# Optimization experiments

Hardware: AMD Instinct MI355X
Metric: run time of the kernel (lower is better)

The kernel has to match this reference:

```python
import jax, jax.numpy as jnp
import numpy as np


def _proj_prelu(x, W, b, a):
    # 1x1 conv (pointwise linear over channels) + PReLU with scalar slope
    y = jnp.einsum('nchw,oc->nohw', x, W) + b[None, :, None, None]
    return jnp.where(y >= 0, y, a[0] * y)


def setup_inputs() -> dict:
    key = jax.random.key(0)
    ks = jax.random.split(key, 8)
    C, Ce = 128, 64
    x = jax.random.normal(ks[0], (4, C, 80, 80), dtype=jnp.float32)
    s = 1.0 / np.sqrt(C)
    Wq = jax.random.normal(ks[1], (Ce, C), dtype=jnp.float32) * s
    bq = jax.random.normal(ks[2], (Ce,), dtype=jnp.float32) * 0.01
    Wk = jax.random.normal(ks[3], (Ce, C), dtype=jnp.float32) * s
    bk = jax.random.normal(ks[4], (Ce,), dtype=jnp.float32) * 0.01
    Wv = jax.random.normal(ks[5], (C, C), dtype=jnp.float32) * s
    bv = jax.random.normal(ks[6], (C,), dtype=jnp.float32) * 0.01
    aq = jnp.full((1,), 0.25, dtype=jnp.float32)
    ak = jnp.full((1,), 0.25, dtype=jnp.float32)
    av = jnp.full((1,), 0.25, dtype=jnp.float32)
    return {'x': x, 'Wq': Wq, 'bq': bq, 'aq': aq, 'Wk': Wk, 'bk': bk,
            'ak': ak, 'Wv': Wv, 'bv': bv, 'av': av}


def reference(x, Wq, bq, aq, Wk, bk, ak, Wv, bv, av):
    q = _proj_prelu(x, Wq, bq, aq)   # [N, Ce, H, W]
    k = _proj_prelu(x, Wk, bk, ak)   # [N, Ce, H, W]
    v = _proj_prelu(x, Wv, bv, av)   # [N, C,  H, W]
    N, Ce, H, W = q.shape
    Cv = v.shape[1]
    HW = H * W
    qf = q.reshape(N, Ce, HW)        # torch permute+view -> [N, HW, Ce] = qf^T
    kf = k.reshape(N, Ce, HW)
    vf = v.reshape(N, Cv, HW)
    score = jnp.einsum('nci,ncj->nij', qf, kf)      # [N, HW, HW]
    attn = jax.nn.softmax(score, axis=2)
    out = jnp.einsum('nij,ncj->nci', attn, vf)      # [N, Cv, HW]
    return out.reshape(N, Cv, H, W)
```

## Files before the change

### kernel.cpp

```cpp
#include <hip/hip_runtime.h>

typedef __attribute__((ext_vector_type(8)))  short bf16x8;
typedef __attribute__((ext_vector_type(16))) float f32x16;
typedef unsigned int u32;
typedef unsigned short u16;

#define HW 6400
#define L2E 1.44269504088896f
#define DEFER_THR 8.0f

__device__ inline u16 f2bf(float f) {
    u32 u = __builtin_bit_cast(u32, f);
    u32 r = (u + 0x7fffu + ((u >> 16) & 1u)) >> 16;
    return (u16)r;
}
__device__ inline u32 cvt_pk_bf16(float lo, float hi) {
    u32 r;
    asm("v_cvt_pk_bf16_f32 %0, %1, %2" : "=v"(r) : "v"(lo), "v"(hi));
    return r;
}
__device__ inline void gload_lds16(const void* g, void* l) {
    __builtin_amdgcn_global_load_lds(
        (const __attribute__((address_space(1))) u32*)g,
        (__attribute__((address_space(3))) u32*)l, 16, 0, 0);
}
__device__ inline float vmax16(const f32x16& v) {
    float a0 = fmaxf(v[0], v[1]),  a1 = fmaxf(v[2], v[3]);
    float a2 = fmaxf(v[4], v[5]),  a3 = fmaxf(v[6], v[7]);
    float a4 = fmaxf(v[8], v[9]),  a5 = fmaxf(v[10], v[11]);
    float a6 = fmaxf(v[12], v[13]), a7 = fmaxf(v[14], v[15]);
    float b0 = fmaxf(a0, a1), b1 = fmaxf(a2, a3);
    float b2 = fmaxf(a4, a5), b3 = fmaxf(a6, a7);
    return fmaxf(fmaxf(b0, b1), fmaxf(b2, b3));
}
__device__ inline float bfpair_sum(u32 w) {
    float hi = __builtin_bit_cast(float, w & 0xFFFF0000u);
    float lo = __builtin_bit_cast(float, w << 16);
    return hi + lo;
}

__global__ __launch_bounds__(256) void proj_kernel(
    const float* __restrict__ x,
    const float* __restrict__ Wq, const float* __restrict__ bq, const float* __restrict__ aq,
    const float* __restrict__ Wk, const float* __restrict__ bk, const float* __restrict__ ak,
    const float* __restrict__ Wv, const float* __restrict__ bv, const float* __restrict__ av,
    u16* __restrict__ QT, u16* __restrict__ KT, u16* __restrict__ Vw)
{
    __shared__ char xs[64 * 272];
    __shared__ char ktr[2][64 * 144];

    const int tid  = threadIdx.x;
    const int lane = tid & 63;
    const int w    = tid >> 6;
    const int l31  = lane & 31;
    const int h    = lane >> 5;

    const int blk = blockIdx.x;
    const int n   = blk / 100;
    const int pt  = blk - n * 100;
    const int p0  = pt * 64;

    const float* xb = x + (size_t)n * 128 * HW + p0;
    #pragma unroll
    for (int it = 0; it < 8; ++it) {
        int idx = it * 256 + tid;
        int c = idx >> 4, p4 = (idx & 15) * 4;
        float4 d = *(const float4*)(xb + (size_t)c * HW + p4);
        *(u16*)(xs + (p4 + 0) * 272 + c * 2) = f2bf(d.x);
        *(u16*)(xs + (p4 + 1) * 272 + c * 2) = f2bf(d.y);
        *(u16*)(xs + (p4 + 2) * 272 + c * 2) = f2bf(d.z);
        *(u16*)(xs + (p4 + 3) * 272 + c * 2) = f2bf(d.w);
    }
    __syncthreads();

    const float* Wsrc; const float* bsrc; float slope; float osc = 1.0f;
    if (w == 0)      { Wsrc = Wq;                 bsrc = bq;             slope = aq[0]; osc = L2E; }
    else if (w == 1) { Wsrc = Wk;                 bsrc = bk;             slope = ak[0]; }
    else             { Wsrc = Wv + (w-2)*64*128;  bsrc = bv + (w-2)*64;  slope = av[0]; }

    bf16x8 wf[2][8];
    #pragma unroll
    for (int cb = 0; cb < 2; ++cb)
        #pragma unroll
        for (int kc = 0; kc < 8; ++kc) {
            const float* ws = Wsrc + (cb * 32 + l31) * 128 + kc * 16 + h * 8;
            float4 a = *(const float4*)ws;
            float4 b = *(const float4*)(ws + 4);
            union { u32 u[4]; bf16x8 v; } uu;
            uu.u[0] = cvt_pk_bf16(a.x, a.y);
            uu.u[1] = cvt_pk_bf16(a.z, a.w);
            uu.u[2] = cvt_pk_bf16(b.x, b.y);
            uu.u[3] = cvt_pk_bf16(b.z, b.w);
            wf[cb][kc] = uu.v;
        }

    f32x16 acc[2][2] = {};
    #pragma unroll
    for (int kc = 0; kc < 8; ++kc) {
        bf16x8 xb0 = *(const bf16x8*)(xs + (l31)      * 272 + kc * 32 + h * 16);
        bf16x8 xb1 = *(const bf16x8*)(xs + (l31 + 32) * 272 + kc * 32 + h * 16);
        acc[0][0] = __builtin_amdgcn_mfma_f32_32x32x16_bf16(wf[0][kc], xb0, acc[0][0], 0, 0, 0);
        acc[0][1] = __builtin_amdgcn_mfma_f32_32x32x16_bf16(wf[0][kc], xb1, acc[0][1], 0, 0, 0);
        acc[1][0] = __builtin_amdgcn_mfma_f32_32x32x16_bf16(wf[1][kc], xb0, acc[1][0], 0, 0, 0);
        acc[1][1] = __builtin_amdgcn_mfma_f32_32x32x16_bf16(wf[1][kc], xb1, acc[1][1], 0, 0, 0);
    }

    if (w >= 2) {
        u16* dst = Vw + ((size_t)n * 128 + (size_t)(w - 2) * 64) * HW;
        #pragma unroll
        for (int cb = 0; cb < 2; ++cb)
            #pragma unroll
            for (int pb = 0; pb < 2; ++pb)
                #pragma unroll
                for (int r = 0; r < 16; ++r) {
                    int ch = cb * 32 + (r & 3) + 8 * (r >> 2) + 4 * h;
                    float y = acc[cb][pb][r] + bsrc[ch];
                    y = (y >= 0.f) ? y : slope * y;
                    dst[(size_t)ch * HW + p0 + pb * 32 + l31] = f2bf(y);
                }
    } else {
        char* tb = ktr[w];
        #pragma unroll
        for (int cb = 0; cb < 2; ++cb)
            #pragma unroll
            for (int pb = 0; pb < 2; ++pb)
                #pragma unroll
                for (int rp = 0; rp < 8; ++rp) {
                    int r0 = rp * 2;
                    int ch = cb * 32 + (r0 & 3) + 8 * (r0 >> 2) + 4 * h;
                    float y0 = acc[cb][pb][r0]     + bsrc[ch];
                    float y1 = acc[cb][pb][r0 + 1] + bsrc[ch + 1];
                    y0 = ((y0 >= 0.f) ? y0 : slope * y0) * osc;
                    y1 = ((y1 >= 0.f) ? y1 : slope * y1) * osc;
                    *(u32*)(tb + (pb * 32 + l31) * 144 + ch * 2) = cvt_pk_bf16(y0, y1);
                }
        u16* dst = (w == 0) ? QT : KT;
        #pragma unroll
        for (int i8 = 0; i8 < 8; ++i8) {
            int p = i8 * 8 + (lane >> 3);
            bf16x8 d = *(const bf16x8*)(tb + p * 144 + (lane & 7) * 16);
            *(bf16x8*)(dst + ((size_t)n * HW + p0 + p) * 64 + (lane & 7) * 8) = d;
        }
    }
}

__global__ __launch_bounds__(256, 2) void attn_kernel(
    const u16* __restrict__ QT, const u16* __restrict__ KT, const u16* __restrict__ Vw,
    float* __restrict__ out,
    float* __restrict__ Opart, float* __restrict__ Mpart, float* __restrict__ Lpart,
    int jsplit, int NT)
{
    __shared__ char lds[49152];

    const int tid  = threadIdx.x;
    const int lane = tid & 63;
    const int w    = tid >> 6;
    const int l31  = lane & 31;
    const int h    = lane >> 5;

    const int per_n = 25 * jsplit;
    const int n    = blockIdx.x / per_n;
    const int rem  = blockIdx.x - n * per_n;
    const int it   = rem / jsplit;
    const int js   = rem - it * jsplit;
    const int i0   = it * 256;
    const int jt0  = js * NT;

    const int rowA = i0 + w * 64 + l31;
    const int rowB = rowA + 32;

    const u16* qbA = QT + ((size_t)n * HW + rowA) * 64;
    bf16x8 qfA[4], qfB[4];
    #pragma unroll
    for (int kc = 0; kc < 4; ++kc) {
        qfA[kc] = *(const bf16x8*)(qbA + kc * 16 + h * 8);
        qfB[kc] = *(const bf16x8*)(qbA + 32 * 64 + kc * 16 + h * 8);
    }

    const char* Kg = (const char*)(KT + (size_t)n * HW * 64);
    const char* Vg = (const char*)(Vw + (size_t)n * 128 * HW);

    auto stage = [&](int buf, int jt) {
        char* B = lds + buf * 24576;
        #pragma unroll
        for (int q = 0; q < 2; ++q) {
            int cc = w + 4 * q;
            gload_lds16(Kg + (size_t)jt * 8192 + lane * 128 + cc * 16, B + cc * 1024);
        }
        #pragma unroll
        for (int q = 0; q < 4; ++q) {
            int v = w + 4 * q;
            int jcc = v >> 1, chalf = v & 1;
            gload_lds16(Vg + (size_t)(chalf * 64 + lane) * 12800 + (size_t)jt * 128 + jcc * 16,
                        B + 8192 + v * 1024);
        }
    };

    f32x16 accA[4] = {}, accB[4] = {};
    float mA = -3e38f, mB = -3e38f, lsA = 0.f, lsB = 0.f;

    auto compute = [&](int buf) {
        char* Klds = lds + buf * 24576;
        char* Vlds = Klds + 8192;

        #pragma unroll
        for (int jb = 0; jb < 2; ++jb) {
            bf16x8 kf[4];
            #pragma unroll
            for (int kc = 0; kc < 4; ++kc)
                kf[kc] = *(const bf16x8*)(Klds + (2 * kc + h) * 1024 + (jb * 32 + l31) * 16);

            __builtin_amdgcn_s_setprio(1);
            f32x16 sA = {}, sB = {};
            #pragma unroll
            for (int kc = 0; kc < 4; ++kc) {
                sA = __builtin_amdgcn_mfma_f32_32x32x16_bf16(kf[kc], qfA[kc], sA, 0, 0, 0);
                sB = __builtin_amdgcn_mfma_f32_32x32x16_bf16(kf[kc], qfB[kc], sB, 0, 0, 0);
            }
            __builtin_amdgcn_s_setprio(0);

            float rmxA = vmax16(sA), rmxB = vmax16(sB);
            rmxA = fmaxf(rmxA, __shfl_xor(rmxA, 32, 64));
            rmxB = fmaxf(rmxB, __shfl_xor(rmxB, 32, 64));

            if (__any(rmxA > mA + DEFER_THR)) {
                float mn = fmaxf(mA, rmxA);
                float a = exp2f(mA - mn);
                lsA *= a;
                #pragma unroll
                for (int cb = 0; cb < 4; ++cb)
                    #pragma unroll
                    for (int r = 0; r < 16; ++r) accA[cb][r] *= a;
                mA = mn;
            }
            if (__any(rmxB > mB + DEFER_THR)) {
                float mn = fmaxf(mB, rmxB);
                float a = exp2f(mB - mn);
                lsB *= a;
                #pragma unroll
                for (int cb = 0; cb < 4; ++cb)
                    #pragma unroll
                    for (int r = 0; r < 16; ++r) accB[cb][r] *= a;
                mB = mn;
            }

            #pragma unroll
            for (int r = 0; r < 16; ++r) {
                sA[r] = exp2f(sA[r] - mA);
                sB[r] = exp2f(sB[r] - mB);
            }

            float rsA = 0.f, rsB = 0.f;
            bf16x8 pfA[2], pfB[2];
            #pragma unroll
            for (int kbl = 0; kbl < 2; ++kbl) {
                const int b = kbl * 8;
                u32 a0 = cvt_pk_bf16(sA[b + 0], sA[b + 1]);
                u32 a1 = cvt_pk_bf16(sA[b + 2], sA[b + 3]);
                u32 a2 = cvt_pk_bf16(sA[b + 4], sA[b + 5]);
                u32 a3 = cvt_pk_bf16(sA[b + 6], sA[b + 7]);
                rsA += (bfpair_sum(a0) + bfpair_sum(a1)) + (bfpair_sum(a2) + bfpair_sum(a3));
                asm("v_permlane32_swap_b32 %0, %1" : "+v"(a0), "+v"(a2));
                asm("v_permlane32_swap_b32 %0, %1" : "+v"(a1), "+v"(a3));
                union { u32 u[4]; bf16x8 v; } ua;
                ua.u[0] = a0; ua.u[1] = a1; ua.u[2] = a2; ua.u[3] = a3;
                pfA[kbl] = ua.v;
                u32 b0 = cvt_pk_bf16(sB[b + 0], sB[b + 1]);
                u32 b1 = cvt_pk_bf16(sB[b + 2], sB[b + 3]);
                u32 b2 = cvt_pk_bf16(sB[b + 4], sB[b + 5]);
                u32 b3 = cvt_pk_bf16(sB[b + 6], sB[b + 7]);
                rsB += (bfpair_sum(b0) + bfpair_sum(b1)) + (bfpair_sum(b2) + bfpair_sum(b3));
                asm("v_permlane32_swap_b32 %0, %1" : "+v"(b0), "+v"(b2));
                asm("v_permlane32_swap_b32 %0, %1" : "+v"(b1), "+v"(b3));
                union { u32 u[4]; bf16x8 v; } ub;
                ub.u[0] = b0; ub.u[1] = b1; ub.u[2] = b2; ub.u[3] = b3;
                pfB[kbl] = ub.v;
            }
            lsA += rsA;
            lsB += rsB;

            __builtin_amdgcn_s_setprio(1);
            #pragma unroll
            for (int kbl = 0; kbl < 2; ++kbl) {
                const int jcc = jb * 4 + 2 * kbl + h;
                #pragma unroll
                for (int cb = 0; cb < 4; ++cb) {
                    bf16x8 vf = *(const bf16x8*)(Vlds + jcc * 2048 + (cb * 32 + l31) * 16);
                    accA[cb] = __builtin_amdgcn_mfma_f32_32x32x16_bf16(vf, pfA[kbl], accA[cb], 0, 0, 0);
                    accB[cb] = __builtin_amdgcn_mfma_f32_32x32x16_bf16(vf, pfB[kbl], accB[cb], 0, 0, 0);
                }
            }
            __builtin_amdgcn_s_setprio(0);
        }
    };

    #define WAITBAR(N) do { \
        asm volatile("s_waitcnt vmcnt(" #N ")" ::: "memory"); \
        __builtin_amdgcn_s_barrier(); \
        __builtin_amdgcn_sched_barrier(0); \
    } while (0)
    #define BAR() do { \
        __builtin_amdgcn_sched_barrier(0); \
        __builtin_amdgcn_s_barrier(); \
        __builtin_amdgcn_sched_barrier(0); \
    } while (0)

    stage(0, jt0);
    int t = 0;
    for (; t + 2 <= NT; t += 2) {
        stage(1, jt0 + t + 1);
        WAITBAR(6);
        compute(0);
        BAR();
        if (t + 2 < NT) {
            stage(0, jt0 + t + 2);
            WAITBAR(6);
        } else {
            WAITBAR(0);
        }
        compute(1);
        BAR();
    }
    if (t < NT) {
        asm volatile("s_waitcnt vmcnt(0)" ::: "memory");
        __builtin_amdgcn_s_barrier();
        __builtin_amdgcn_sched_barrier(0);
        compute(0);
    }
    #undef WAITBAR
    #undef BAR

    lsA += __shfl_xor(lsA, 32, 64);
    lsB += __shfl_xor(lsB, 32, 64);

    if (Opart != nullptr) {
        float* Ob = Opart + (size_t)(js * 4 + n) * 128 * HW;
        #pragma unroll
        for (int cb = 0; cb < 4; ++cb)
            #pragma unroll
            for (int r = 0; r < 16; ++r) {
                int c = cb * 32 + (r & 3) + 8 * (r >> 2) + 4 * h;
                Ob[(size_t)c * HW + rowA] = accA[cb][r];
                Ob[(size_t)c * HW + rowB] = accB[cb][r];
            }
        if (h == 0) {
            Mpart[(size_t)(js * 4 + n) * HW + rowA] = mA;
            Mpart[(size_t)(js * 4 + n) * HW + rowB] = mB;
            Lpart[(size_t)(js * 4 + n) * HW + rowA] = lsA;
            Lpart[(size_t)(js * 4 + n) * HW + rowB] = lsB;
        }
    } else {
        float invA = 1.f / lsA, invB = 1.f / lsB;
        float* ob = out + (size_t)n * 128 * HW;
        #pragma unroll
        for (int cb = 0; cb < 4; ++cb)
            #pragma unroll
            for (int r = 0; r < 16; ++r) {
                int c = cb * 32 + (r & 3) + 8 * (r >> 2) + 4 * h;
                ob[(size_t)c * HW + rowA] = accA[cb][r] * invA;
                ob[(size_t)c * HW + rowB] = accB[cb][r] * invB;
            }
    }
}

__global__ __launch_bounds__(256) void combine_kernel(
    const float* __restrict__ Opart, const float* __restrict__ Mpart,
    const float* __restrict__ Lpart, float* __restrict__ out, int jsplit)
{
    const int b = blockIdx.x;
    const int n = b / 100;
    const int rem = b - n * 100;
    const int cq = rem / 25;
    const int ic = rem - cq * 25;
    const int i = ic * 256 + threadIdx.x;

    float mj[5], wj[5];
    float M = -3e38f;
    #pragma unroll
    for (int js = 0; js < 5; ++js) {
        mj[js] = (js < jsplit) ? Mpart[(size_t)(js * 4 + n) * HW + i] : -3e38f;
        M = fmaxf(M, mj[js]);
    }
    float L = 0.f;
    #pragma unroll
    for (int js = 0; js < 5; ++js) {
        wj[js] = (js < jsplit) ? exp2f(mj[js] - M) : 0.f;
        if (js < jsplit) L += Lpart[(size_t)(js * 4 + n) * HW + i] * wj[js];
    }
    const float inv = 1.f / L;

    for (int c = cq * 32; c < cq * 32 + 32; ++c) {
        float acc = 0.f;
        #pragma unroll
        for (int js = 0; js < 5; ++js)
            if (js < jsplit)
                acc += Opart[((size_t)(js * 4 + n) * 128 + c) * HW + i] * wj[js];
        out[((size_t)n * 128 + c) * HW + i] = acc * inv;
    }
}

extern "C" void kernel_launch(void* const* d_in, const int* in_sizes, int n_in,
                              void* d_out, int out_size, void* d_ws, size_t ws_size,
                              hipStream_t stream) {
    const float* x  = (const float*)d_in[0];
    const float* Wq = (const float*)d_in[1];
    const float* bq = (const float*)d_in[2];
    const float* aq = (const float*)d_in[3];
    const float* Wk = (const float*)d_in[4];
    const float* bk = (const float*)d_in[5];
    const float* ak = (const float*)d_in[6];
    const float* Wv = (const float*)d_in[7];
    const float* bv = (const float*)d_in[8];
    const float* av = (const float*)d_in[9];

    char* wsp = (char*)d_ws;
    u16* QT  = (u16*)wsp;
    u16* KT  = (u16*)(wsp + 3276800);
    u16* Vw  = (u16*)(wsp + 6553600);
    const size_t base = 13107200;
    const size_t oslab = 13107200;
    const size_t mslab = 102400;

    proj_kernel<<<dim3(400), 256, 0, stream>>>(x, Wq, bq, aq, Wk, bk, ak, Wv, bv, av,
                                               QT, KT, Vw);

    int jsplit = 0;
    for (int js = 5; js >= 4; --js) {
        size_t need = base + (size_t)js * (oslab + 2 * mslab);
        if (ws_size >= need) { jsplit = js; break; }
    }

    if (jsplit > 0) {
        float* Opart = (float*)(wsp + base);
        float* Mpart = (float*)(wsp + base + (size_t)jsplit * oslab);
        float* Lpart = (float*)(wsp + base + (size_t)jsplit * (oslab + mslab));
        int NT = 100 / jsplit;
        attn_kernel<<<dim3(4 * 25 * jsplit), 256, 0, stream>>>(QT, KT, Vw, (float*)d_out,
                                                               Opart, Mpart, Lpart, jsplit, NT);
        combine_kernel<<<dim3(400), 256, 0, stream>>>(Opart, Mpart, Lpart, (float*)d_out, jsplit);
    } else {
        attn_kernel<<<dim3(100), 256, 0, stream>>>(QT, KT, Vw, (float*)d_out,
                                                   nullptr, nullptr, nullptr, 1, 100);
    }
}
```

Before: 167.0 us.

## Use raw exp2 intrinsic, sum fp32 probabilities directly, retune LDS pitches

Replaces exp2f with the hardware exp2 intrinsic in the attention and combine kernels, which drops the denormal/range fixup code around each exponential. The row sum is now taken from the fp32 probabilities instead of unpacking the bf16-packed pairs. The LDS row pitches in the projection kernel change from 272/144 to 260/132 bytes to alter the bank mapping. The new pitches are not multiples of 16, so the 16-byte vector LDS reads lose alignment. The row sum may also differ slightly from the bf16 values actually fed to the PV matmul.

New measurement: 143.7 us. 1.16x faster.

```diff
diff --git a/kernel.cpp b/kernel.cpp
--- a/kernel.cpp
+++ b/kernel.cpp
@@ -8,6 +8,8 @@
 #define HW 6400
 #define L2E 1.44269504088896f
 #define DEFER_THR 8.0f
+#define XPITCH 260
+#define KPITCH 132
 
 __device__ inline u16 f2bf(float f) {
     u32 u = __builtin_bit_cast(u32, f);
@@ -33,10 +35,13 @@
     float b2 = fmaxf(a4, a5), b3 = fmaxf(a6, a7);
     return fmaxf(fmaxf(b0, b1), fmaxf(b2, b3));
 }
-__device__ inline float bfpair_sum(u32 w) {
-    float hi = __builtin_bit_cast(float, w & 0xFFFF0000u);
-    float lo = __builtin_bit_cast(float, w << 16);
-    return hi + lo;
+__device__ inline float vsum16(const f32x16& v) {
+    float a0 = v[0] + v[1],  a1 = v[2] + v[3];
+    float a2 = v[4] + v[5],  a3 = v[6] + v[7];
+    float a4 = v[8] + v[9],  a5 = v[10] + v[11];
+    float a6 = v[12] + v[13], a7 = v[14] + v[15];
+    float b0 = a0 + a1, b1 = a2 + a3, b2 = a4 + a5, b3 = a6 + a7;
+    return (b0 + b1) + (b2 + b3);
 }
 
 __global__ __launch_bounds__(256) void proj_kernel(
@@ -46,8 +51,8 @@
     const float* __restrict__ Wv, const float* __restrict__ bv, const float* __restrict__ av,
     u16* __restrict__ QT, u16* __restrict__ KT, u16* __restrict__ Vw)
 {
-    __shared__ char xs[64 * 272];
-    __shared__ char ktr[2][64 * 144];
+    __shared__ char xs[64 * XPITCH];
+    __shared__ char ktr[2][64 * KPITCH];
 
     const int tid  = threadIdx.x;
     const int lane = tid & 63;
@@ -66,10 +71,10 @@
         int idx = it * 256 + tid;
         int c = idx >> 4, p4 = (idx & 15) * 4;
         float4 d = *(const float4*)(xb + (size_t)c * HW + p4);
-        *(u16*)(xs + (p4 + 0) * 272 + c * 2) = f2bf(d.x);
-        *(u16*)(xs + (p4 + 1) * 272 + c * 2) = f2bf(d.y);
-        *(u16*)(xs + (p4 + 2) * 272 + c * 2) = f2bf(d.z);
-        *(u16*)(xs + (p4 + 3) * 272 + c * 2) = f2bf(d.w);
+        *(u16*)(xs + (p4 + 0) * XPITCH + c * 2) = f2bf(d.x);
+        *(u16*)(xs + (p4 + 1) * XPITCH + c * 2) = f2bf(d.y);
+        *(u16*)(xs + (p4 + 2) * XPITCH + c * 2) = f2bf(d.z);
+        *(u16*)(xs + (p4 + 3) * XPITCH + c * 2) = f2bf(d.w);
     }
     __syncthreads();
 
@@ -97,8 +102,8 @@
     f32x16 acc[2][2] = {};
     #pragma unroll
     for (int kc = 0; kc < 8; ++kc) {
-        bf16x8 xb0 = *(const bf16x8*)(xs + (l31)      * 272 + kc * 32 + h * 16);
-        bf16x8 xb1 = *(const bf16x8*)(xs + (l31 + 32) * 272 + kc * 32 + h * 16);
+        bf16x8 xb0 = *(const bf16x8*)(xs + (l31)      * XPITCH + kc * 32 + h * 16);
+        bf16x8 xb1 = *(const bf16x8*)(xs + (l31 + 32) * XPITCH + kc * 32 + h * 16);
         acc[0][0] = __builtin_amdgcn_mfma_f32_32x32x16_bf16(wf[0][kc], xb0, acc[0][0], 0, 0, 0);
         acc[0][1] = __builtin_amdgcn_mfma_f32_32x32x16_bf16(wf[0][kc], xb1, acc[0][1], 0, 0, 0);
         acc[1][0] = __builtin_amdgcn_mfma_f32_32x32x16_bf16(wf[1][kc], xb0, acc[1][0], 0, 0, 0);
@@ -132,13 +137,13 @@
                     float y1 = acc[cb][pb][r0 + 1] + bsrc[ch + 1];
                     y0 = ((y0 >= 0.f) ? y0 : slope * y0) * osc;
                     y1 = ((y1 >= 0.f) ? y1 : slope * y1) * osc;
-                    *(u32*)(tb + (pb * 32 + l31) * 144 + ch * 2) = cvt_pk_bf16(y0, y1);
+                    *(u32*)(tb + (pb * 32 + l31) * KPITCH + ch * 2) = cvt_pk_bf16(y0, y1);
                 }
         u16* dst = (w == 0) ? QT : KT;
         #pragma unroll
         for (int i8 = 0; i8 < 8; ++i8) {
             int p = i8 * 8 + (lane >> 3);
-            bf16x8 d = *(const bf16x8*)(tb + p * 144 + (lane & 7) * 16);
+            bf16x8 d = *(const bf16x8*)(tb + p * KPITCH + (lane & 7) * 16);
             *(bf16x8*)(dst + ((size_t)n * HW + p0 + p) * 64 + (lane & 7) * 8) = d;
         }
     }
@@ -225,7 +230,7 @@
 
             if (__any(rmxA > mA + DEFER_THR)) {
                 float mn = fmaxf(mA, rmxA);
-                float a = exp2f(mA - mn);
+                float a = __builtin_amdgcn_exp2f(mA - mn);
                 lsA *= a;
                 #pragma unroll
                 for (int cb = 0; cb < 4; ++cb)
@@ -235,7 +240,7 @@
             }
             if (__any(rmxB > mB + DEFER_THR)) {
                 float mn = fmaxf(mB, rmxB);
-                float a = exp2f(mB - mn);
+                float a = __builtin_amdgcn_exp2f(mB - mn);
                 lsB *= a;
                 #pragma unroll
                 for (int cb = 0; cb < 4; ++cb)
@@ -246,11 +251,12 @@
 
             #pragma unroll
             for (int r = 0; r < 16; ++r) {
-                sA[r] = exp2f(sA[r] - mA);
-                sB[r] = exp2f(sB[r] - mB);
-            }
-
-            float rsA = 0.f, rsB = 0.f;
+                sA[r] = __builtin_amdgcn_exp2f(sA[r] - mA);
+                sB[r] = __builtin_amdgcn_exp2f(sB[r] - mB);
+            }
+            lsA += vsum16(sA);
+            lsB += vsum16(sB);
+
             bf16x8 pfA[2], pfB[2];
             #pragma unroll
             for (int kbl = 0; kbl < 2; ++kbl) {
@@ -259,7 +265,6 @@
                 u32 a1 = cvt_pk_bf16(sA[b + 2], sA[b + 3]);
                 u32 a2 = cvt_pk_bf16(sA[b + 4], sA[b + 5]);
                 u32 a3 = cvt_pk_bf16(sA[b + 6], sA[b + 7]);
-                rsA += (bfpair_sum(a0) + bfpair_sum(a1)) + (bfpair_sum(a2) + bfpair_sum(a3));
                 asm("v_permlane32_swap_b32 %0, %1" : "+v"(a0), "+v"(a2));
                 asm("v_permlane32_swap_b32 %0, %1" : "+v"(a1), "+v"(a3));
                 union { u32 u[4]; bf16x8 v; } ua;
@@ -269,15 +274,12 @@
                 u32 b1 = cvt_pk_bf16(sB[b + 2], sB[b + 3]);
                 u32 b2 = cvt_pk_bf16(sB[b + 4], sB[b + 5]);
                 u32 b3 = cvt_pk_bf16(sB[b + 6], sB[b + 7]);
-                rsB += (bfpair_sum(b0) + bfpair_sum(b1)) + (bfpair_sum(b2) + bfpair_sum(b3));
                 asm("v_permlane32_swap_b32 %0, %1" : "+v"(b0), "+v"(b2));
                 asm("v_permlane32_swap_b32 %0, %1" : "+v"(b1), "+v"(b3));
                 union { u32 u[4]; bf16x8 v; } ub;
                 ub.u[0] = b0; ub.u[1] = b1; ub.u[2] = b2; ub.u[3] = b3;
                 pfB[kbl] = ub.v;
             }
-            lsA += rsA;
-            lsB += rsB;
 
             __builtin_amdgcn_s_setprio(1);
             #pragma unroll
@@ -384,7 +386,7 @@
     float L = 0.f;
     #pragma unroll
     for (int js = 0; js < 5; ++js) {
-        wj[js] = (js < jsplit) ? exp2f(mj[js] - M) : 0.f;
+        wj[js] = (js < jsplit) ? __builtin_amdgcn_exp2f(mj[js] - M) : 0.f;
         if (js < jsplit) L += Lpart[(size_t)(js * 4 + n) * HW + i] * wj[js];
     }
     const float inv = 1.f / L;
```
